# Performance work log

Measured on AMD Instinct MI355X. Metric: run time of the kernel, lower is better.

## Reference

```python
import jax, jax.numpy as jnp
import numpy as np

D = 768      # feature_dim
HD = 768     # hidden_dim
NH = 4       # num_heads
B, T1, T2 = 4, 128, 128
LN_EPS = 1e-5

def setup_inputs() -> dict:
    key = jax.random.key(0)
    ks = jax.random.split(key, 12)
    s = 0.02
    return {
        'speech_features': jax.random.normal(ks[0], (B, T1, D), jnp.float32),
        'phoneme_features': jax.random.normal(ks[1], (B, T2, D), jnp.float32),
        # per-head attention MLP: Linear(2D->HD), ReLU, Linear(HD->1); stacked over heads
        'W1': jax.random.normal(ks[2], (NH, 2 * D, HD), jnp.float32) * s,
        'b1': jnp.zeros((NH, HD), jnp.float32),
        'w2': jax.random.normal(ks[3], (NH, HD), jnp.float32) * s,
        'b2': jnp.zeros((NH,), jnp.float32),
        # fusion: Linear(2D->2HD), ReLU, Linear(2HD->D), LayerNorm(D)
        'Wf1': jax.random.normal(ks[4], (2 * D, 2 * HD), jnp.float32) * s,
        'bf1': jnp.zeros((2 * HD,), jnp.float32),
        'Wf2': jax.random.normal(ks[5], (2 * HD, D), jnp.float32) * s,
        'bf2': jnp.zeros((D,), jnp.float32),
        'ln_g': jnp.ones((D,), jnp.float32),
        'ln_b': jnp.zeros((D,), jnp.float32),
    }

def reference(speech_features, phoneme_features, W1, b1, w2, b2, Wf1, bf1, Wf2, bf2, ln_g, ln_b):
    d = speech_features.shape[-1]
    # Decompose Linear(cat([speech_t, phoneme])) = speech@W1[:d] + phoneme@W1[d:] + b1
    Wx, Wy = W1[:, :d, :], W1[:, d:, :]
    sx = jnp.einsum('btd,ndh->nbth', speech_features, Wx)   # [NH,B,T1,HD]
    py = jnp.einsum('bsd,ndh->nbsh', phoneme_features, Wy)  # [NH,B,T2,HD]
    hidden = jax.nn.relu(sx[:, :, :, None, :] + py[:, :, None, :, :]
                         + b1[:, None, None, None, :])      # [NH,B,T1,T2,HD]
    scores = jnp.einsum('nbtsh,nh->nbts', hidden, w2) + b2[:, None, None, None]
    attn = jax.nn.softmax(scores, axis=-1).mean(axis=0)     # [B,T1,T2]
    context = jnp.einsum('bts,bsd->btd', attn, phoneme_features)  # [B,T1,D]
    fused = jnp.concatenate([speech_features, context], axis=-1)  # [B,T1,2D]
    # dropout is identity in eval mode
    h = jax.nn.relu(fused @ Wf1 + bf1)
    out = h @ Wf2 + bf2
    mu = out.mean(axis=-1, keepdims=True)
    var = ((out - mu) ** 2).mean(axis=-1, keepdims=True)
    out = (out - mu) * jax.lax.rsqrt(var + LN_EPS) * ln_g + ln_b
    return out.mean(axis=1)  # [B,D]
```

## Files before the change

### kernel.cpp

```cpp
#include <hip/hip_runtime.h>
#include <cstddef>


#define D_  768
#define HD_ 768
#define NH_ 4
#define B_  4
#define T1_ 128
#define T2_ 128
#define M_  (B_*T1_)
#define LN_EPS_ 1e-5f

typedef unsigned short u16;
typedef _Float16 f16;
typedef _Float16 f16x2 __attribute__((ext_vector_type(2)));
typedef __bf16 bf16x8 __attribute__((ext_vector_type(8)));
typedef float f32x4 __attribute__((ext_vector_type(4)));

__device__ __forceinline__ u16 f2bf(float f) {
    union { float f; unsigned int u; } v; v.f = f;
    unsigned int u = v.u + (0x7FFFu + ((v.u >> 16) & 1u));
    return (u16)(u >> 16);
}
__device__ __forceinline__ f16x2 bcast2(unsigned int u) {
    return __builtin_bit_cast(f16x2, u);
}
__device__ __forceinline__ u16 f16bits(f16 h) {
    return __builtin_bit_cast(unsigned short, h);
}

template<bool RELU, int MODE>
__device__ __forceinline__ void gemm_mfma_body(
    const u16* __restrict__ A, int lda,
    const u16* __restrict__ Bt, int ldb,
    const float* __restrict__ bias,
    void* __restrict__ C, int ldc, int K, int m0, int n0)
{
    __shared__ __align__(16) u16 As[64][40];
    __shared__ __align__(16) u16 Bs[64][40];

    const int tid = threadIdx.x;
    const int row = tid >> 2;
    const int kq  = (tid & 3) << 3;
    const int lane = tid & 63;
    const int w  = tid >> 6;
    const int wr = (w >> 1) << 5;
    const int wc = (w & 1) << 5;
    const int l16 = lane & 15;
    const int lk8 = (lane >> 4) << 3;
    const int r4  = (lane >> 4) << 2;

    const u16* aptr = A + (size_t)(m0 + row) * lda + kq;
    const u16* bptr = Bt + (size_t)(n0 + row) * ldb + kq;

    f32x4 acc00 = {0.f,0.f,0.f,0.f}, acc01 = {0.f,0.f,0.f,0.f};
    f32x4 acc10 = {0.f,0.f,0.f,0.f}, acc11 = {0.f,0.f,0.f,0.f};

    uint4 a_nxt = *(const uint4*)aptr;
    uint4 b_nxt = *(const uint4*)bptr;

    for (int k0 = 0; k0 < K; k0 += 32) {
        __syncthreads();
        *(uint4*)&As[row][kq] = a_nxt;
        *(uint4*)&Bs[row][kq] = b_nxt;
        if (k0 + 32 < K) {
            a_nxt = *(const uint4*)(aptr + k0 + 32);
            b_nxt = *(const uint4*)(bptr + k0 + 32);
        }
        __syncthreads();
        bf16x8 af0 = *(const bf16x8*)&As[wr + l16][lk8];
        bf16x8 af1 = *(const bf16x8*)&As[wr + 16 + l16][lk8];
        bf16x8 bf0 = *(const bf16x8*)&Bs[wc + l16][lk8];
        bf16x8 bf1 = *(const bf16x8*)&Bs[wc + 16 + l16][lk8];
        acc00 = __builtin_amdgcn_mfma_f32_16x16x32_bf16(af0, bf0, acc00, 0, 0, 0);
        acc01 = __builtin_amdgcn_mfma_f32_16x16x32_bf16(af0, bf1, acc01, 0, 0, 0);
        acc10 = __builtin_amdgcn_mfma_f32_16x16x32_bf16(af1, bf0, acc10, 0, 0, 0);
        acc11 = __builtin_amdgcn_mfma_f32_16x16x32_bf16(af1, bf1, acc11, 0, 0, 0);
    }

#define EPI_FRAG(ACC, MF, NF)                                                  \
    {                                                                          \
        const int gcol = n0 + wc + (NF)*16 + l16;                              \
        const float bv = bias ? bias[gcol] : 0.f;                              \
        float v_[4];                                                           \
        _Pragma("unroll")                                                      \
        for (int r = 0; r < 4; r++) {                                          \
            float v = ACC[r] + bv;                                             \
            if (RELU) v = fmaxf(v, 0.f);                                       \
            v_[r] = v;                                                         \
        }                                                                      \
        const int grow0 = m0 + wr + (MF)*16 + r4;                              \
        if (MODE == 3) {                                                       \
             \
            u16* dst = (u16*)C + (size_t)(grow0 >> 7) * (768 * 128)            \
                     + (size_t)gcol * 128 + (grow0 & 127);                     \
            ushort4 pk4;                                                       \
            pk4.x = f16bits((f16)v_[0]); pk4.y = f16bits((f16)v_[1]);          \
            pk4.z = f16bits((f16)v_[2]); pk4.w = f16bits((f16)v_[3]);          \
            *(ushort4*)dst = pk4;                                              \
        } else {                                                               \
            _Pragma("unroll")                                                  \
            for (int r = 0; r < 4; r++) {                                      \
                const size_t off = (size_t)(grow0 + r) * ldc + gcol;           \
                if (MODE == 0) ((float*)C)[off] = v_[r];                       \
                else if (MODE == 1) ((u16*)C)[off] = f2bf(v_[r]);              \
                else ((u16*)C)[off] = f16bits((f16)v_[r]);                     \
            }                                                                  \
        }                                                                      \
    }
    EPI_FRAG(acc00, 0, 0) EPI_FRAG(acc01, 0, 1)
    EPI_FRAG(acc10, 1, 0) EPI_FRAG(acc11, 1, 1)
#undef EPI_FRAG
}

__global__ void convert_bf16_kernel(const float* __restrict__ s, const float* __restrict__ p,
                                    u16* __restrict__ so, u16* __restrict__ po)
{
    const float* in = blockIdx.y ? p : s;
    u16* out = blockIdx.y ? po : so;
    const int i = (blockIdx.x * 256 + threadIdx.x) * 4;
    float4 v = *(const float4*)(in + i);
    ushort4 o;
    o.x = f2bf(v.x); o.y = f2bf(v.y); o.z = f2bf(v.z); o.w = f2bf(v.w);
    *(ushort4*)(out + i) = o;
}

__global__ void transpose_convert_kernel(const float* __restrict__ W1,
                                         const float* __restrict__ Wf1,
                                         const float* __restrict__ Wf2,
                                         u16* __restrict__ w1t,
                                         u16* __restrict__ wf1t,
                                         u16* __restrict__ wf2t)
{
    const int z = blockIdx.z;
    const float* in; u16* out; int C;
    if (z < 4)       { in = W1 + (size_t)z * 1536 * 768; out = w1t + (size_t)z * 768 * 1536; C = 768; }
    else if (z == 4) { in = Wf1; out = wf1t; C = 1536; }
    else             { in = Wf2; out = wf2t; C = 768; }
    const int c0 = blockIdx.x * 32, r0 = blockIdx.y * 32;
    if (c0 >= C) return;
    __shared__ float tile[32][33];
    const int t = threadIdx.x;
    const int tr = t >> 3, tc = (t & 7) << 2;
    float4 v = *(const float4*)(in + (size_t)(r0 + tr) * C + c0 + tc);
    tile[tr][tc] = v.x; tile[tr][tc + 1] = v.y; tile[tr][tc + 2] = v.z; tile[tr][tc + 3] = v.w;
    __syncthreads();
    ushort4 o;
    o.x = f2bf(tile[tc + 0][tr]); o.y = f2bf(tile[tc + 1][tr]);
    o.z = f2bf(tile[tc + 2][tr]); o.w = f2bf(tile[tc + 3][tr]);
    *(ushort4*)(out + (size_t)(c0 + tr) * 1536 + r0 + tc) = o;
}

__global__ void gemm_sxpy_kernel(const u16* __restrict__ sp, const u16* __restrict__ ph,
                                 const u16* __restrict__ w1t, const float* __restrict__ b1,
                                 u16* __restrict__ sxf, u16* __restrict__ pyt)
{
    const int z = blockIdx.z;
    const int n = z & 3;
    const bool ispy = z >= 4;
    const u16* Bt = w1t + (size_t)n * 768 * 1536 + (ispy ? 768 : 0);
    if (!ispy) {
        gemm_mfma_body<false, 2>(sp, 768, Bt, 1536, b1 + n * HD_,
                                 sxf + (size_t)n * M_ * HD_, HD_, 768,
                                 blockIdx.y * 64, blockIdx.x * 64);
    } else {
        gemm_mfma_body<false, 3>(ph, 768, Bt, 1536, nullptr,
                                 pyt + (size_t)n * 4 * 768 * 128, 0, 768,
                                 blockIdx.y * 64, blockIdx.x * 64);
    }
}

template<bool RELU, int MODE>
__global__ void gemm_mfma_kernel(const u16* __restrict__ A, int lda,
                                 const u16* __restrict__ Bt, int ldb,
                                 const float* __restrict__ bias,
                                 void* __restrict__ C, int ldc, int K)
{
    gemm_mfma_body<RELU, MODE>(A, lda, Bt, ldb, bias, C, ldc, K,
                               blockIdx.y * 64, blockIdx.x * 64);
}

__global__ __launch_bounds__(256) void scores_softmax_kernel(
    const u16* __restrict__ sxf,
    const u16* __restrict__ pyt,
    const float* __restrict__ w2,
    float* __restrict__ probs)
{
    const int bid = blockIdx.x;
    const int n = bid >> 6, b = (bid >> 4) & 3, t0 = (bid & 15) * 8;
    const int tid = threadIdx.x, lane = tid & 63, w = tid >> 6;

    __shared__ __align__(16) f16x2 sxs[8][768];
    __shared__ __align__(16) f16x2 w2s[768];

    for (int q = 0; q < 6; q++) {
        const int u = tid + q * 256;
        const int r = u / 192;
        const int h4 = (u % 192) * 4;
        ushort4 v = *(const ushort4*)(sxf + ((size_t)(n * 512 + b * 128 + t0 + r)) * 768 + h4);
        sxs[r][h4 + 0] = bcast2((unsigned)v.x * 0x10001u);
        sxs[r][h4 + 1] = bcast2((unsigned)v.y * 0x10001u);
        sxs[r][h4 + 2] = bcast2((unsigned)v.z * 0x10001u);
        sxs[r][h4 + 3] = bcast2((unsigned)v.w * 0x10001u);
    }
    for (int q = 0; q < 3; q++) {
        const int i = tid + q * 256;
        f16 hv = (f16)w2[n * 768 + i];
        f16x2 s2; s2.x = hv; s2.y = hv;
        w2s[i] = s2;
    }
    __syncthreads();

    const f16x2* pypanel = (const f16x2*)(pyt + ((size_t)((n << 2) | b)) * 768 * 128) + lane;

    float accA0 = 0.f, accA1 = 0.f, accB0 = 0.f, accB1 = 0.f;
    const int rA = 2 * w, rB = 2 * w + 1;

    f16x2 b0[16], b1[16];
#pragma unroll
    for (int j = 0; j < 16; j++) b0[j] = pypanel[(size_t)j * 64];
#pragma unroll
    for (int j = 0; j < 16; j++) b1[j] = pypanel[(size_t)(16 + j) * 64];

    auto compute = [&](const f16x2 (&buf)[16], int hbase) {
        f16x2 aA = {(f16)0, (f16)0}, aB = {(f16)0, (f16)0};
#pragma unroll
        for (int j4 = 0; j4 < 16; j4 += 4) {
            uint4 sau = *(const uint4*)&sxs[rA][hbase + j4];
            uint4 sbu = *(const uint4*)&sxs[rB][hbase + j4];
            uint4 wvu = *(const uint4*)&w2s[hbase + j4];
            const unsigned sa_[4] = {sau.x, sau.y, sau.z, sau.w};
            const unsigned sb_[4] = {sbu.x, sbu.y, sbu.z, sbu.w};
            const unsigned wv_[4] = {wvu.x, wvu.y, wvu.z, wvu.w};
#pragma unroll
            for (int j = 0; j < 4; j++) {
                const f16x2 p = buf[j4 + j];
                const f16x2 wj = bcast2(wv_[j]);
                const f16x2 z = {(f16)0, (f16)0};
                f16x2 ra = __builtin_elementwise_max(bcast2(sa_[j]) + p, z);
                f16x2 rb = __builtin_elementwise_max(bcast2(sb_[j]) + p, z);
                aA = __builtin_elementwise_fma(ra, wj, aA);
                aB = __builtin_elementwise_fma(rb, wj, aB);
            }
        }
        accA0 += (float)aA.x; accA1 += (float)aA.y;
        accB0 += (float)aB.x; accB1 += (float)aB.y;
    };

    for (int hc = 0; hc < 768; hc += 32) {
        compute(b0, hc);
        if (hc + 32 < 768) {
#pragma unroll
            for (int j = 0; j < 16; j++) b0[j] = pypanel[(size_t)(hc + 32 + j) * 64];
        }
        compute(b1, hc + 16);
        if (hc + 48 < 768) {
#pragma unroll
            for (int j = 0; j < 16; j++) b1[j] = pypanel[(size_t)(hc + 48 + j) * 64];
        }
    }

#pragma unroll
    for (int which = 0; which < 2; which++) {
        const float s0 = which ? accB0 : accA0;
        const float s1 = which ? accB1 : accA1;
        const int t = t0 + 2 * w + which;
        float mx = fmaxf(s0, s1);
#pragma unroll
        for (int off = 32; off; off >>= 1) mx = fmaxf(mx, __shfl_xor(mx, off, 64));
        const float e0 = expf(s0 - mx), e1 = expf(s1 - mx);
        float sm = e0 + e1;
#pragma unroll
        for (int off = 32; off; off >>= 1) sm += __shfl_xor(sm, off, 64);
        const float inv = 0.25f / sm;
        float2 pr; pr.x = e0 * inv; pr.y = e1 * inv;
        *(float2*)&probs[((size_t)(n * 512 + b * 128 + t)) * 128 + 2 * lane] = pr;
    }
}

__global__ void context_fused_kernel(const float* __restrict__ probs,
                                     const float* __restrict__ phon,
                                     const float* __restrict__ speech,
                                     u16* __restrict__ fused)
{
    const int m = blockIdx.x;
    const int b = m >> 7;
    const int tid = threadIdx.x;
    __shared__ float attn[T2_];
    if (tid < T2_) {
        float a = 0.f;
#pragma unroll
        for (int n = 0; n < NH_; n++)
            a += probs[(size_t)(n * M_ + m) * T2_ + tid];
        attn[tid] = a;
    }
    __syncthreads();
    const float* ph = phon + (size_t)b * T2_ * D_;
#pragma unroll
    for (int j = 0; j < 3; j++) {
        const int d = tid + 256 * j;
        float acc = 0.f;
#pragma unroll 8
        for (int s = 0; s < T2_; s++)
            acc = fmaf(attn[s], ph[(size_t)s * D_ + d], acc);
        fused[(size_t)m * (2 * D_) + d] = f2bf(speech[(size_t)m * D_ + d]);
        fused[(size_t)m * (2 * D_) + D_ + d] = f2bf(acc);
    }
}

__global__ void ln_stats_kernel(const float* __restrict__ x,
                                float* __restrict__ mu, float* __restrict__ rsig)
{
    const int row = blockIdx.x * 4 + (threadIdx.x >> 6);
    const int lane = threadIdx.x & 63;
    const float4* x4 = (const float4*)(x + (size_t)row * D_);
    float s = 0.f, ss = 0.f;
#pragma unroll
    for (int j = 0; j < 3; j++) {
        float4 v = x4[j * 64 + lane];
        s += v.x + v.y + v.z + v.w;
        ss += v.x * v.x + v.y * v.y + v.z * v.z + v.w * v.w;
    }
#pragma unroll
    for (int off = 32; off; off >>= 1) {
        s += __shfl_xor(s, off, 64);
        ss += __shfl_xor(ss, off, 64);
    }
    if (lane == 0) {
        const float m_ = s * (1.f / D_);
        const float var = ss * (1.f / D_) - m_ * m_;
        mu[row] = m_;
        rsig[row] = rsqrtf(var + LN_EPS_);
    }
}

__global__ void ln_mean_kernel(const float* __restrict__ x,
                               const float* __restrict__ mu,
                               const float* __restrict__ rsig,
                               const float* __restrict__ g,
                               const float* __restrict__ lb,
                               float* __restrict__ out)
{
    const int b = blockIdx.x;
    const int tid = threadIdx.x;
    __shared__ float rs[T1_];
    __shared__ float red[256];
    float pr = 0.f;
    if (tid < T1_) {
        const float r = rsig[b * T1_ + tid];
        rs[tid] = r;
        pr = mu[b * T1_ + tid] * r;
    }
    red[tid] = pr;
    __syncthreads();
    for (int st = 128; st; st >>= 1) {
        if (tid < st) red[tid] += red[tid + st];
        __syncthreads();
    }
    const float S = red[0];
    const float* xb = x + (size_t)b * T1_ * D_;
#pragma unroll
    for (int j = 0; j < 3; j++) {
        const int d = tid + 256 * j;
        float acc = 0.f;
#pragma unroll 8
        for (int t = 0; t < T1_; t++)
            acc = fmaf(xb[(size_t)t * D_ + d], rs[t], acc);
        out[b * D_ + d] = g[d] * (acc - S) * (1.f / T1_) + lb[d];
    }
}

extern "C" void kernel_launch(void* const* d_in, const int* in_sizes, int n_in,
                              void* d_out, int out_size, void* d_ws, size_t ws_size,
                              hipStream_t stream)
{
    const float* speech = (const float*)d_in[0];
    const float* phon   = (const float*)d_in[1];
    const float* W1     = (const float*)d_in[2];
    const float* b1     = (const float*)d_in[3];
    const float* w2     = (const float*)d_in[4];
    const float* Wf1    = (const float*)d_in[6];
    const float* bf1    = (const float*)d_in[7];
    const float* Wf2    = (const float*)d_in[8];
    const float* bf2    = (const float*)d_in[9];
    const float* ln_g   = (const float*)d_in[10];
    const float* ln_b   = (const float*)d_in[11];
    float* out = (float*)d_out;

    char* w = (char*)d_ws;
    auto alloc = [&](size_t bytes) { char* p = w; w += (bytes + 1023) & ~(size_t)1023; return p; };
    u16* sp_bf  = (u16*)alloc((size_t)M_ * D_ * 2);
    u16* ph_bf  = (u16*)alloc((size_t)M_ * D_ * 2);
    u16* w1t    = (u16*)alloc((size_t)NH_ * 768 * 1536 * 2);
    u16* wf1t   = (u16*)alloc((size_t)1536 * 1536 * 2);
    u16* wf2t   = (u16*)alloc((size_t)768 * 1536 * 2);
    u16* sxf    = (u16*)alloc((size_t)NH_ * M_ * HD_ * 2);
    u16* pyt    = (u16*)alloc((size_t)NH_ * B_ * 768 * 128 * 2);
    float* probs  = (float*)alloc((size_t)NH_ * M_ * T2_ * 4);
    u16* fusedb = (u16*)alloc((size_t)M_ * 2 * D_ * 2);
    u16* hbuf   = (u16*)alloc((size_t)M_ * 2 * HD_ * 2);
    float* outpre = (float*)alloc((size_t)M_ * D_ * 4);
    float* mub    = (float*)alloc(M_ * 4);
    float* rsigb  = (float*)alloc(M_ * 4);

    hipLaunchKernelGGL(convert_bf16_kernel, dim3(384, 2), dim3(256), 0, stream,
                       speech, phon, sp_bf, ph_bf);
    hipLaunchKernelGGL(transpose_convert_kernel, dim3(48, 48, 6), dim3(256), 0, stream,
                       W1, Wf1, Wf2, w1t, wf1t, wf2t);
    hipLaunchKernelGGL(gemm_sxpy_kernel, dim3(HD_ / 64, M_ / 64, 8), dim3(256), 0, stream,
                       sp_bf, ph_bf, w1t, b1, sxf, pyt);
    hipLaunchKernelGGL(scores_softmax_kernel, dim3(256), dim3(256), 0, stream,
                       sxf, pyt, w2, probs);
    hipLaunchKernelGGL(context_fused_kernel, dim3(M_), dim3(256), 0, stream,
                       probs, phon, speech, fusedb);
    hipLaunchKernelGGL((gemm_mfma_kernel<true, 1>), dim3(2 * HD_ / 64, M_ / 64), dim3(256), 0, stream,
                       fusedb, 2 * D_, wf1t, 1536, bf1, hbuf, 2 * HD_, 2 * D_);
    hipLaunchKernelGGL((gemm_mfma_kernel<false, 0>), dim3(D_ / 64, M_ / 64), dim3(256), 0, stream,
                       hbuf, 2 * HD_, wf2t, 1536, bf2, outpre, D_, 2 * HD_);
    hipLaunchKernelGGL(ln_stats_kernel, dim3(M_ / 4), dim3(256), 0, stream,
                       outpre, mub, rsigb);
    hipLaunchKernelGGL(ln_mean_kernel, dim3(B_), dim3(256), 0, stream,
                       outpre, mub, rsigb, ln_g, ln_b, out);
}
```

Before: 130.3 us.

## Merge prep and LayerNorm kernels, stage transposed py stores, hand-code packed f16 scoring

The bf16 conversion and weight-transpose kernels are merged into one flat-grid prep kernel, and the LayerNorm stats and mean kernels are merged into one kernel per batch. The transposed py store in the GEMM epilogue now goes through shared memory so global writes are coalesced. The score inner loop uses inline v_pk_add/max/fma f16 asm with one u32 LDS read per element instead of uint4 loads, and launch bounds are added. Fewer launches cut launch overhead, but the fused LN kernel runs the row statistics on only 4 blocks, which serializes that work.

```diff
diff --git a/kernel.cpp b/kernel.cpp
--- a/kernel.cpp
+++ b/kernel.cpp
@@ -12,6 +12,7 @@
 #define LN_EPS_ 1e-5f
 
 typedef unsigned short u16;
+typedef unsigned int u32;
 typedef _Float16 f16;
 typedef _Float16 f16x2 __attribute__((ext_vector_type(2)));
 typedef __bf16 bf16x8 __attribute__((ext_vector_type(8)));
@@ -22,11 +23,26 @@
     unsigned int u = v.u + (0x7FFFu + ((v.u >> 16) & 1u));
     return (u16)(u >> 16);
 }
-__device__ __forceinline__ f16x2 bcast2(unsigned int u) {
-    return __builtin_bit_cast(f16x2, u);
-}
 __device__ __forceinline__ u16 f16bits(f16 h) {
     return __builtin_bit_cast(unsigned short, h);
+}
+__device__ __forceinline__ u32 splat2(u16 h) {
+    return (u32)h * 0x10001u;
+}
+__device__ __forceinline__ u32 pk_add(u32 a, u32 b) {
+    u32 d; asm("v_pk_add_f16 %0, %1, %2" : "=v"(d) : "v"(a), "v"(b)); return d;
+}
+__device__ __forceinline__ u32 pk_max0(u32 a) {
+    u32 d; asm("v_pk_max_f16 %0, %1, %2" : "=v"(d) : "v"(a), "v"(0u)); return d;
+}
+__device__ __forceinline__ u32 pk_fma(u32 a, u32 b, u32 c) {
+    u32 d; asm("v_pk_fma_f16 %0, %1, %2, %3" : "=v"(d) : "v"(a), "v"(b), "v"(c)); return d;
+}
+__device__ __forceinline__ float lo_f(u32 u) {
+    f16x2 v = __builtin_bit_cast(f16x2, u); return (float)v.x;
+}
+__device__ __forceinline__ float hi_f(u32 u) {
+    f16x2 v = __builtin_bit_cast(f16x2, u); return (float)v.y;
 }
 
 template<bool RELU, int MODE>
@@ -38,6 +54,7 @@
 {
     __shared__ __align__(16) u16 As[64][40];
     __shared__ __align__(16) u16 Bs[64][40];
+    __shared__ u16 Ts[MODE == 3 ? 64 : 1][MODE == 3 ? 68 : 1];
 
     const int tid = threadIdx.x;
     const int row = tid >> 2;
@@ -89,19 +106,15 @@
             if (RELU) v = fmaxf(v, 0.f);                                       \
             v_[r] = v;                                                         \
         }                                                                      \
-        const int grow0 = m0 + wr + (MF)*16 + r4;                              \
+        const int lr0 = wr + (MF)*16 + r4;                                     \
         if (MODE == 3) {                                                       \
-             \
-            u16* dst = (u16*)C + (size_t)(grow0 >> 7) * (768 * 128)            \
-                     + (size_t)gcol * 128 + (grow0 & 127);                     \
-            ushort4 pk4;                                                       \
-            pk4.x = f16bits((f16)v_[0]); pk4.y = f16bits((f16)v_[1]);          \
-            pk4.z = f16bits((f16)v_[2]); pk4.w = f16bits((f16)v_[3]);          \
-            *(ushort4*)dst = pk4;                                              \
+            const int lc = wc + (NF)*16 + l16;                                 \
+            _Pragma("unroll")                                                  \
+            for (int r = 0; r < 4; r++) Ts[lc][lr0 + r] = f16bits((f16)v_[r]); \
         } else {                                                               \
             _Pragma("unroll")                                                  \
             for (int r = 0; r < 4; r++) {                                      \
-                const size_t off = (size_t)(grow0 + r) * ldc + gcol;           \
+                const size_t off = (size_t)(m0 + lr0 + r) * ldc + gcol;        \
                 if (MODE == 0) ((float*)C)[off] = v_[r];                       \
                 else if (MODE == 1) ((u16*)C)[off] = f2bf(v_[r]);              \
                 else ((u16*)C)[off] = f16bits((f16)v_[r]);                     \
@@ -111,49 +124,75 @@
     EPI_FRAG(acc00, 0, 0) EPI_FRAG(acc01, 0, 1)
     EPI_FRAG(acc10, 1, 0) EPI_FRAG(acc11, 1, 1)
 #undef EPI_FRAG
-}
-
-__global__ void convert_bf16_kernel(const float* __restrict__ s, const float* __restrict__ p,
-                                    u16* __restrict__ so, u16* __restrict__ po)
-{
-    const float* in = blockIdx.y ? p : s;
-    u16* out = blockIdx.y ? po : so;
-    const int i = (blockIdx.x * 256 + threadIdx.x) * 4;
-    float4 v = *(const float4*)(in + i);
-    ushort4 o;
-    o.x = f2bf(v.x); o.y = f2bf(v.y); o.z = f2bf(v.z); o.w = f2bf(v.w);
-    *(ushort4*)(out + i) = o;
-}
-
-__global__ void transpose_convert_kernel(const float* __restrict__ W1,
-                                         const float* __restrict__ Wf1,
-                                         const float* __restrict__ Wf2,
-                                         u16* __restrict__ w1t,
-                                         u16* __restrict__ wf1t,
-                                         u16* __restrict__ wf2t)
-{
-    const int z = blockIdx.z;
-    const float* in; u16* out; int C;
-    if (z < 4)       { in = W1 + (size_t)z * 1536 * 768; out = w1t + (size_t)z * 768 * 1536; C = 768; }
-    else if (z == 4) { in = Wf1; out = wf1t; C = 1536; }
-    else             { in = Wf2; out = wf2t; C = 768; }
-    const int c0 = blockIdx.x * 32, r0 = blockIdx.y * 32;
-    if (c0 >= C) return;
+
+    if (MODE == 3) {
+        __syncthreads();
+        u16* cb = (u16*)C + (size_t)(m0 >> 7) * (768 * 128) + (m0 & 127);
+#pragma unroll
+        for (int u = 0; u < 4; u++) {
+            const int i = tid + u * 256;
+            const int hl = i >> 4;
+            const int s4 = (i & 15) << 2;
+            ushort4 o;
+            o.x = Ts[hl][s4 + 0]; o.y = Ts[hl][s4 + 1];
+            o.z = Ts[hl][s4 + 2]; o.w = Ts[hl][s4 + 3];
+            *(ushort4*)(cb + (size_t)(n0 + hl) * 128 + s4) = o;
+        }
+    }
+}
+
+__global__ __launch_bounds__(256) void prep_kernel(
+    const float* __restrict__ speech, const float* __restrict__ phon,
+    const float* __restrict__ W1, const float* __restrict__ Wf1,
+    const float* __restrict__ Wf2,
+    u16* __restrict__ spb, u16* __restrict__ phb,
+    u16* __restrict__ w1t, u16* __restrict__ wf1t, u16* __restrict__ wf2t)
+{
+    const int tid = threadIdx.x;
+    int bid = blockIdx.x;
+    if (bid < 768) {
+        const bool isp = bid < 384;
+        const float* in = isp ? speech : phon;
+        u16* outb = isp ? spb : phb;
+        const int i = ((isp ? bid : bid - 384) * 256 + tid) * 4;
+        float4 v = *(const float4*)(in + i);
+        ushort4 o;
+        o.x = f2bf(v.x); o.y = f2bf(v.y); o.z = f2bf(v.z); o.w = f2bf(v.w);
+        *(ushort4*)(outb + i) = o;
+        return;
+    }
+    bid -= 768;
+    const float* in; u16* outp; int tx, ty;
+    if (bid < 4608) {
+        const int z = bid / 1152, r = bid % 1152;
+        tx = r % 24; ty = r / 24;
+        in = W1 + (size_t)z * 1536 * 768; outp = w1t + (size_t)z * 768 * 1536;
+    } else if (bid < 6912) {
+        const int r = bid - 4608;
+        tx = r % 48; ty = r / 48;
+        in = Wf1; outp = wf1t;
+    } else {
+        const int r = bid - 6912;
+        tx = r % 24; ty = r / 24;
+        in = Wf2; outp = wf2t;
+    }
+    const int C = (bid >= 4608 && bid < 6912) ? 1536 : 768;
+    const int c0 = tx * 32, r0 = ty * 32;
     __shared__ float tile[32][33];
-    const int t = threadIdx.x;
-    const int tr = t >> 3, tc = (t & 7) << 2;
+    const int tr = tid >> 3, tc = (tid & 7) << 2;
     float4 v = *(const float4*)(in + (size_t)(r0 + tr) * C + c0 + tc);
     tile[tr][tc] = v.x; tile[tr][tc + 1] = v.y; tile[tr][tc + 2] = v.z; tile[tr][tc + 3] = v.w;
     __syncthreads();
     ushort4 o;
     o.x = f2bf(tile[tc + 0][tr]); o.y = f2bf(tile[tc + 1][tr]);
     o.z = f2bf(tile[tc + 2][tr]); o.w = f2bf(tile[tc + 3][tr]);
-    *(ushort4*)(out + (size_t)(c0 + tr) * 1536 + r0 + tc) = o;
-}
-
-__global__ void gemm_sxpy_kernel(const u16* __restrict__ sp, const u16* __restrict__ ph,
-                                 const u16* __restrict__ w1t, const float* __restrict__ b1,
-                                 u16* __restrict__ sxf, u16* __restrict__ pyt)
+    *(ushort4*)(outp + (size_t)(c0 + tr) * 1536 + r0 + tc) = o;
+}
+
+__global__ __launch_bounds__(256) void gemm_sxpy_kernel(
+    const u16* __restrict__ sp, const u16* __restrict__ ph,
+    const u16* __restrict__ w1t, const float* __restrict__ b1,
+    u16* __restrict__ sxf, u16* __restrict__ pyt)
 {
     const int z = blockIdx.z;
     const int n = z & 3;
@@ -171,10 +210,11 @@
 }
 
 template<bool RELU, int MODE>
-__global__ void gemm_mfma_kernel(const u16* __restrict__ A, int lda,
-                                 const u16* __restrict__ Bt, int ldb,
-                                 const float* __restrict__ bias,
-                                 void* __restrict__ C, int ldc, int K)
+__global__ __launch_bounds__(256) void gemm_mfma_kernel(
+    const u16* __restrict__ A, int lda,
+    const u16* __restrict__ Bt, int ldb,
+    const float* __restrict__ bias,
+    void* __restrict__ C, int ldc, int K)
 {
     gemm_mfma_body<RELU, MODE>(A, lda, Bt, ldb, bias, C, ldc, K,
                                blockIdx.y * 64, blockIdx.x * 64);
@@ -190,61 +230,47 @@
     const int n = bid >> 6, b = (bid >> 4) & 3, t0 = (bid & 15) * 8;
     const int tid = threadIdx.x, lane = tid & 63, w = tid >> 6;
 
-    __shared__ __align__(16) f16x2 sxs[8][768];
-    __shared__ __align__(16) f16x2 w2s[768];
+    __shared__ __align__(16) u32 sxs[8][768];
+    __shared__ __align__(16) u32 w2s[768];
 
     for (int q = 0; q < 6; q++) {
         const int u = tid + q * 256;
         const int r = u / 192;
         const int h4 = (u % 192) * 4;
         ushort4 v = *(const ushort4*)(sxf + ((size_t)(n * 512 + b * 128 + t0 + r)) * 768 + h4);
-        sxs[r][h4 + 0] = bcast2((unsigned)v.x * 0x10001u);
-        sxs[r][h4 + 1] = bcast2((unsigned)v.y * 0x10001u);
-        sxs[r][h4 + 2] = bcast2((unsigned)v.z * 0x10001u);
-        sxs[r][h4 + 3] = bcast2((unsigned)v.w * 0x10001u);
+        sxs[r][h4 + 0] = splat2(v.x);
+        sxs[r][h4 + 1] = splat2(v.y);
+        sxs[r][h4 + 2] = splat2(v.z);
+        sxs[r][h4 + 3] = splat2(v.w);
     }
     for (int q = 0; q < 3; q++) {
         const int i = tid + q * 256;
-        f16 hv = (f16)w2[n * 768 + i];
-        f16x2 s2; s2.x = hv; s2.y = hv;
-        w2s[i] = s2;
+        w2s[i] = splat2(f16bits((f16)w2[n * 768 + i]));
     }
     __syncthreads();
 
-    const f16x2* pypanel = (const f16x2*)(pyt + ((size_t)((n << 2) | b)) * 768 * 128) + lane;
+    const u32* pypanel = (const u32*)(pyt + ((size_t)((n << 2) | b)) * 768 * 128) + lane;
 
     float accA0 = 0.f, accA1 = 0.f, accB0 = 0.f, accB1 = 0.f;
     const int rA = 2 * w, rB = 2 * w + 1;
 
-    f16x2 b0[16], b1[16];
+    u32 b0[16], b1[16];
 #pragma unroll
     for (int j = 0; j < 16; j++) b0[j] = pypanel[(size_t)j * 64];
 #pragma unroll
     for (int j = 0; j < 16; j++) b1[j] = pypanel[(size_t)(16 + j) * 64];
 
-    auto compute = [&](const f16x2 (&buf)[16], int hbase) {
-        f16x2 aA = {(f16)0, (f16)0}, aB = {(f16)0, (f16)0};
-#pragma unroll
-        for (int j4 = 0; j4 < 16; j4 += 4) {
-            uint4 sau = *(const uint4*)&sxs[rA][hbase + j4];
-            uint4 sbu = *(const uint4*)&sxs[rB][hbase + j4];
-            uint4 wvu = *(const uint4*)&w2s[hbase + j4];
-            const unsigned sa_[4] = {sau.x, sau.y, sau.z, sau.w};
-            const unsigned sb_[4] = {sbu.x, sbu.y, sbu.z, sbu.w};
-            const unsigned wv_[4] = {wvu.x, wvu.y, wvu.z, wvu.w};
-#pragma unroll
-            for (int j = 0; j < 4; j++) {
-                const f16x2 p = buf[j4 + j];
-                const f16x2 wj = bcast2(wv_[j]);
-                const f16x2 z = {(f16)0, (f16)0};
-                f16x2 ra = __builtin_elementwise_max(bcast2(sa_[j]) + p, z);
-                f16x2 rb = __builtin_elementwise_max(bcast2(sb_[j]) + p, z);
-                aA = __builtin_elementwise_fma(ra, wj, aA);
-                aB = __builtin_elementwise_fma(rb, wj, aB);
-            }
-        }
-        accA0 += (float)aA.x; accA1 += (float)aA.y;
-        accB0 += (float)aB.x; accB1 += (float)aB.y;
+    auto compute = [&](const u32 (&buf)[16], int hbase) {
+        u32 aA = 0u, aB = 0u;
+#pragma unroll
+        for (int j = 0; j < 16; j++) {
+            const u32 p = buf[j];
+            const u32 wj = w2s[hbase + j];
+            aA = pk_fma(pk_max0(pk_add(sxs[rA][hbase + j], p)), wj, aA);
+            aB = pk_fma(pk_max0(pk_add(sxs[rB][hbase + j], p)), wj, aB);
+        }
+        accA0 += lo_f(aA); accA1 += hi_f(aA);
+        accB0 += lo_f(aB); accB1 += hi_f(aB);
     };
 
     for (int hc = 0; hc < 768; hc += 32) {
@@ -278,10 +304,9 @@
     }
 }
 
-__global__ void context_fused_kernel(const float* __restrict__ probs,
-                                     const float* __restrict__ phon,
-                                     const float* __restrict__ speech,
-                                     u16* __restrict__ fused)
+__global__ __launch_bounds__(256) void context_fused_kernel(
+    const float* __restrict__ probs, const float* __restrict__ phon,
+    const float* __restrict__ speech, u16* __restrict__ fused)
 {
     const int m = blockIdx.x;
     const int b = m >> 7;
@@ -308,56 +333,41 @@
     }
 }
 
-__global__ void ln_stats_kernel(const float* __restrict__ x,
-                                float* __restrict__ mu, float* __restrict__ rsig)
-{
-    const int row = blockIdx.x * 4 + (threadIdx.x >> 6);
-    const int lane = threadIdx.x & 63;
-    const float4* x4 = (const float4*)(x + (size_t)row * D_);
-    float s = 0.f, ss = 0.f;
-#pragma unroll
-    for (int j = 0; j < 3; j++) {
-        float4 v = x4[j * 64 + lane];
-        s += v.x + v.y + v.z + v.w;
-        ss += v.x * v.x + v.y * v.y + v.z * v.z + v.w * v.w;
-    }
-#pragma unroll
-    for (int off = 32; off; off >>= 1) {
-        s += __shfl_xor(s, off, 64);
-        ss += __shfl_xor(ss, off, 64);
-    }
-    if (lane == 0) {
-        const float m_ = s * (1.f / D_);
-        const float var = ss * (1.f / D_) - m_ * m_;
-        mu[row] = m_;
-        rsig[row] = rsqrtf(var + LN_EPS_);
-    }
-}
-
-__global__ void ln_mean_kernel(const float* __restrict__ x,
-                               const float* __restrict__ mu,
-                               const float* __restrict__ rsig,
-                               const float* __restrict__ g,
-                               const float* __restrict__ lb,
-                               float* __restrict__ out)
-{
-    const int b = blockIdx.x;
-    const int tid = threadIdx.x;
+__global__ __launch_bounds__(256) void ln_fused_kernel(
+    const float* __restrict__ x, const float* __restrict__ g,
+    const float* __restrict__ lb, float* __restrict__ out)
+{
+    const int b = blockIdx.x, tid = threadIdx.x, lane = tid & 63, w = tid >> 6;
     __shared__ float rs[T1_];
-    __shared__ float red[256];
-    float pr = 0.f;
-    if (tid < T1_) {
-        const float r = rsig[b * T1_ + tid];
-        rs[tid] = r;
-        pr = mu[b * T1_ + tid] * r;
-    }
-    red[tid] = pr;
+    __shared__ float Sred[4];
+
+    float prsum = 0.f;
+    for (int i = 0; i < 32; i++) {
+        const int row = w * 32 + i;
+        const float4* x4 = (const float4*)(x + ((size_t)(b * T1_ + row)) * D_);
+        float s = 0.f, ss = 0.f;
+#pragma unroll
+        for (int j = 0; j < 3; j++) {
+            float4 v = x4[j * 64 + lane];
+            s += v.x + v.y + v.z + v.w;
+            ss += v.x * v.x + v.y * v.y + v.z * v.z + v.w * v.w;
+        }
+#pragma unroll
+        for (int off = 32; off; off >>= 1) {
+            s += __shfl_xor(s, off, 64);
+            ss += __shfl_xor(ss, off, 64);
+        }
+        if (lane == 0) {
+            const float mu = s * (1.f / D_);
+            const float var = ss * (1.f / D_) - mu * mu;
+            const float r = rsqrtf(var + LN_EPS_);
+            rs[row] = r;
+            prsum += mu * r;
+        }
+    }
+    if (lane == 0) Sred[w] = prsum;
     __syncthreads();
-    for (int st = 128; st; st >>= 1) {
-        if (tid < st) red[tid] += red[tid + st];
-        __syncthreads();
-    }
-    const float S = red[0];
+    const float S = Sred[0] + Sred[1] + Sred[2] + Sred[3];
     const float* xb = x + (size_t)b * T1_ * D_;
 #pragma unroll
     for (int j = 0; j < 3; j++) {
@@ -400,13 +410,9 @@
     u16* fusedb = (u16*)alloc((size_t)M_ * 2 * D_ * 2);
     u16* hbuf   = (u16*)alloc((size_t)M_ * 2 * HD_ * 2);
     float* outpre = (float*)alloc((size_t)M_ * D_ * 4);
-    float* mub    = (float*)alloc(M_ * 4);
-    float* rsigb  = (float*)alloc(M_ * 4);
-
-    hipLaunchKernelGGL(convert_bf16_kernel, dim3(384, 2), dim3(256), 0, stream,
-                       speech, phon, sp_bf, ph_bf);
-    hipLaunchKernelGGL(transpose_convert_kernel, dim3(48, 48, 6), dim3(256), 0, stream,
-                       W1, Wf1, Wf2, w1t, wf1t, wf2t);
+
+    hipLaunchKernelGGL(prep_kernel, dim3(8832), dim3(256), 0, stream,
+                       speech, phon, W1, Wf1, Wf2, sp_bf, ph_bf, w1t, wf1t, wf2t);
     hipLaunchKernelGGL(gemm_sxpy_kernel, dim3(HD_ / 64, M_ / 64, 8), dim3(256), 0, stream,
                        sp_bf, ph_bf, w1t, b1, sxf, pyt);
     hipLaunchKernelGGL(scores_softmax_kernel, dim3(256), dim3(256), 0, stream,
@@ -417,8 +423,6 @@
                        fusedb, 2 * D_, wf1t, 1536, bf1, hbuf, 2 * HD_, 2 * D_);
     hipLaunchKernelGGL((gemm_mfma_kernel<false, 0>), dim3(D_ / 64, M_ / 64), dim3(256), 0, stream,
                        hbuf, 2 * HD_, wf2t, 1536, bf2, outpre, D_, 2 * HD_);
-    hipLaunchKernelGGL(ln_stats_kernel, dim3(M_ / 4), dim3(256), 0, stream,
-                       outpre, mub, rsigb);
-    hipLaunchKernelGGL(ln_mean_kernel, dim3(B_), dim3(256), 0, stream,
-                       outpre, mub, rsigb, ln_g, ln_b, out);
-}
+    hipLaunchKernelGGL(ln_fused_kernel, dim3(B_), dim3(256), 0, stream,
+                       outpre, ln_g, ln_b, out);
+}
```

Measured after the change: 141.6 us. 8.7% more time.
